# Kernel optimization log

Hardware: AMD Instinct MI355X
Metric: run time of the kernel (lower is better)

## Reference

```python
import jax, jax.numpy as jnp
import numpy as np

B, T, D = 2, 1024, 1024
H, HKV = 16, 4
HD = D // H            # 64, head dim
GROUPS = H // HKV      # 4
E, K, F = 32, 4, 256   # experts, top-k, expert hidden
FS = 2 * F             # shared expert hidden = n_shared_experts * expert_dim
ROPE_THETA = 500000.0


def rmsnorm(x, w, eps=1e-6):
    return x * jax.lax.rsqrt(jnp.mean(x * x, axis=-1, keepdims=True) + eps) * w


def apply_rope(x, cos, sin):
    # x: (B, T, H, HD); pairs of adjacent features form complex numbers
    xr = x.reshape(*x.shape[:-1], -1, 2)
    a, b = xr[..., 0], xr[..., 1]
    c = cos[None, :, None, :]
    s = sin[None, :, None, :]
    out = jnp.stack([a * c - b * s, a * s + b * c], axis=-1)
    return out.reshape(x.shape)


def setup_inputs():
    key = jax.random.key(0)
    ks = jax.random.split(key, 14)
    # RoPE phasors (real/imag of freqs_cis), shape (T, HD//2)
    inv = 1.0 / (ROPE_THETA ** (np.arange(0, HD, 2, dtype=np.float32) / HD))
    ang = np.arange(T, dtype=np.float32)[:, None] * inv[None, :]
    n = lambda k, shape, d: (jax.random.normal(k, shape, jnp.float32) / np.sqrt(d))
    return {
        "x": jax.random.normal(ks[0], (B, T, D), jnp.float32),
        "freqs_cos": jnp.asarray(np.cos(ang)),
        "freqs_sin": jnp.asarray(np.sin(ang)),
        "norm1_w": jnp.ones((D,), jnp.float32),
        "norm2_w": jnp.ones((D,), jnp.float32),
        "wq": n(ks[1], (D, H * HD), D),
        "wk": n(ks[2], (D, HKV * HD), D),
        "wv": n(ks[3], (D, HKV * HD), D),
        "wo": n(ks[4], (H * HD, D), H * HD),
        "router_w": n(ks[5], (D, E), D),
        "w_gate": n(ks[6], (E, D, F), D),
        "w_up": n(ks[7], (E, D, F), D),
        "w_down": n(ks[8], (E, F, D), F),
        "sh_gate": n(ks[9], (D, FS), D),
        "sh_up": n(ks[10], (D, FS), D),
        "sh_down": n(ks[11], (FS, D), FS),
    }


def reference(x, freqs_cos, freqs_sin, norm1_w, norm2_w, wq, wk, wv, wo,
              router_w, w_gate, w_up, w_down, sh_gate, sh_up, sh_down):
    # ---- GQA attention (pre-norm, residual), eval mode, causal ----
    h = rmsnorm(x, norm1_w)
    q = (h @ wq).reshape(B, T, H, HD)
    k = (h @ wk).reshape(B, T, HKV, HD)
    v = (h @ wv).reshape(B, T, HKV, HD)
    q = apply_rope(q, freqs_cos, freqs_sin)
    k = apply_rope(k, freqs_cos, freqs_sin)
    k = jnp.repeat(k, GROUPS, axis=2)   # (B, T, H, HD)
    v = jnp.repeat(v, GROUPS, axis=2)
    scores = jnp.einsum("bqhd,bkhd->bhqk", q, k) * (HD ** -0.5)
    causal = jnp.tril(jnp.ones((T, T), bool))
    scores = jnp.where(causal[None, None], scores, jnp.finfo(scores.dtype).min)
    probs = jax.nn.softmax(scores, axis=-1)
    attn = jnp.einsum("bhqk,bkhd->bqhd", probs, v).reshape(B, T, H * HD)
    x = x + attn @ wo

    # ---- top-K routed MoE SwiGLU FFN + shared expert (pre-norm, residual) ----
    h = rmsnorm(x, norm2_w).reshape(-1, D)              # (N, D)
    gate_scores = jax.nn.softmax(h @ router_w, axis=-1) # (N, E)
    top_vals, top_idx = jax.lax.top_k(gate_scores, K)   # (N, K)
    combine = jnp.sum(jax.nn.one_hot(top_idx, E, dtype=h.dtype) * top_vals[..., None], axis=1)  # (N, E)
    g = jnp.einsum("nd,edf->nef", h, w_gate)
    u = jnp.einsum("nd,edf->nef", h, w_up)
    hh = jax.nn.silu(g) * u * combine[:, :, None]       # combine-masked: only top-K experts contribute
    routed = jnp.einsum("nef,efd->nd", hh, w_down)
    shared = (jax.nn.silu(h @ sh_gate) * (h @ sh_up)) @ sh_down
    return x + (routed + shared).reshape(B, T, D)
```

## Files before the change

kernel.cpp:

```cpp
#include <hip/hip_runtime.h>

typedef unsigned short u16;
typedef _Float16 h8v __attribute__((ext_vector_type(8)));
typedef __attribute__((ext_vector_type(4))) float f4v;

#define DEV static __device__ __forceinline__

DEV u16 f2h(float f) {
  union { _Float16 h; u16 u; } v; v.h = (_Float16)f; return v.u;
}
DEV float h2f(u16 u) {
  union { u16 u; _Float16 h; } v; v.u = u; return (float)v.h;
}

DEV f4v mfma16h(h8v a, h8v b, f4v c) {
  return __builtin_amdgcn_mfma_f32_16x16x32_f16(a, b, c, 0, 0, 0);
}

__global__ __launch_bounds__(256) void prep_kernel(
    const float* __restrict__ wq, const float* __restrict__ wk,
    const float* __restrict__ wv, const float* __restrict__ wo,
    const float* __restrict__ shg, const float* __restrict__ shu,
    const float* __restrict__ shd,
    const float* __restrict__ wg, const float* __restrict__ wu,
    const float* __restrict__ wd,
    u16* __restrict__ wqkvT, u16* __restrict__ woT, u16* __restrict__ shguT,
    u16* __restrict__ shdT, u16* __restrict__ wguT, u16* __restrict__ wdT,
    const float* __restrict__ x, const float* __restrict__ n1w,
    u16* __restrict__ hH, int* __restrict__ counts) {
  int blk = blockIdx.x;
  if (blk < 7168) {
    const float* in; u16* out; int R, C, gx, gy; long long ozs; int base;
    if (blk < 256)       { in=wq;  out=wqkvT;                    R=1024; C=1024; gx=16; gy=16; ozs=0;        base=0; }
    else if (blk < 320)  { in=wk;  out=wqkvT+(size_t)1024*1024;  R=1024; C=256;  gx=4;  gy=16; ozs=0;        base=256; }
    else if (blk < 384)  { in=wv;  out=wqkvT+(size_t)1280*1024;  R=1024; C=256;  gx=4;  gy=16; ozs=0;        base=320; }
    else if (blk < 640)  { in=wo;  out=woT;                      R=1024; C=1024; gx=16; gy=16; ozs=0;        base=384; }
    else if (blk < 768)  { in=shg; out=shguT;                    R=1024; C=512;  gx=8;  gy=16; ozs=0;        base=640; }
    else if (blk < 896)  { in=shu; out=shguT+(size_t)512*1024;   R=1024; C=512;  gx=8;  gy=16; ozs=0;        base=768; }
    else if (blk < 1024) { in=shd; out=shdT;                     R=512;  C=1024; gx=16; gy=8;  ozs=0;        base=896; }
    else if (blk < 3072) { in=wg;  out=wguT;                     R=1024; C=256;  gx=4;  gy=16; ozs=512*1024; base=1024; }
    else if (blk < 5120) { in=wu;  out=wguT+(size_t)256*1024;    R=1024; C=256;  gx=4;  gy=16; ozs=512*1024; base=3072; }
    else                 { in=wd;  out=wdT;                      R=256;  C=1024; gx=16; gy=4;  ozs=256*1024; base=5120; }
    int i = blk - base;
    int bx = i % gx; int rem = i / gx; int by = rem % gy; int z = rem / gy;
    __shared__ float tile[64][65];
    const float* inp = in + (size_t)z * R * C;
    u16* op = out + (size_t)z * ozs;
    int c0 = bx * 64, r0 = by * 64;
    int tcol = (threadIdx.x & 15) * 4;
    int trow = threadIdx.x >> 4;
    #pragma unroll
    for (int p = 0; p < 4; ++p) {
      int row = trow + p*16;
      float4 v = *(const float4*)(inp + (size_t)(r0+row)*C + c0 + tcol);
      tile[row][tcol] = v.x; tile[row][tcol+1] = v.y;
      tile[row][tcol+2] = v.z; tile[row][tcol+3] = v.w;
    }
    __syncthreads();
    int tcol8 = (threadIdx.x & 7) * 8;
    int trow2 = threadIdx.x >> 3;
    #pragma unroll
    for (int p = 0; p < 2; ++p) {
      int c = trow2 + p*32;
      uint4 ov;
      ov.x = (unsigned)f2h(tile[tcol8+0][c]) | ((unsigned)f2h(tile[tcol8+1][c]) << 16);
      ov.y = (unsigned)f2h(tile[tcol8+2][c]) | ((unsigned)f2h(tile[tcol8+3][c]) << 16);
      ov.z = (unsigned)f2h(tile[tcol8+4][c]) | ((unsigned)f2h(tile[tcol8+5][c]) << 16);
      ov.w = (unsigned)f2h(tile[tcol8+6][c]) | ((unsigned)f2h(tile[tcol8+7][c]) << 16);
      *(uint4*)(op + (size_t)(c0+c)*R + r0 + tcol8) = ov;
    }
  } else if (blk < 9216) {
    int n = blk - 7168;
    int t = threadIdx.x;
    const float* xr = x + (size_t)n * 1024;
    float4 v = ((const float4*)xr)[t];
    float ss = v.x*v.x + v.y*v.y + v.z*v.z + v.w*v.w;
    #pragma unroll
    for (int o = 1; o < 64; o <<= 1) ss += __shfl_xor(ss, o, 64);
    __shared__ float wsum[4];
    if ((t & 63) == 0) wsum[t >> 6] = ss;
    __syncthreads();
    float tot = wsum[0] + wsum[1] + wsum[2] + wsum[3];
    float rs = rsqrtf(tot * (1.0f/1024.0f) + 1e-6f);
    float4 wv4 = ((const float4*)n1w)[t];
    ushort4 oh = { f2h(v.x*rs*wv4.x), f2h(v.y*rs*wv4.y),
                   f2h(v.z*rs*wv4.z), f2h(v.w*rs*wv4.w) };
    ((ushort4*)(hH + (size_t)n*1024))[t] = oh;
  } else {
    if (threadIdx.x < 32) counts[threadIdx.x] = 0;
  }
}

__global__ __launch_bounds__(256) void rmsnorm_kernel(const float* __restrict__ xin,
                                                      const float* __restrict__ w,
                                                      u16* __restrict__ outH,
                                                      float* __restrict__ outF) {
  int n = blockIdx.x;
  int t = threadIdx.x;
  const float* xr = xin + (size_t)n * 1024;
  float4 v = ((const float4*)xr)[t];
  float ss = v.x*v.x + v.y*v.y + v.z*v.z + v.w*v.w;
  #pragma unroll
  for (int o = 1; o < 64; o <<= 1) ss += __shfl_xor(ss, o, 64);
  __shared__ float wsum[4];
  if ((t & 63) == 0) wsum[t >> 6] = ss;
  __syncthreads();
  float tot = wsum[0] + wsum[1] + wsum[2] + wsum[3];
  float rs = rsqrtf(tot * (1.0f/1024.0f) + 1e-6f);
  float4 wv = ((const float4*)w)[t];
  float o0 = v.x*rs*wv.x, o1 = v.y*rs*wv.y, o2 = v.z*rs*wv.z, o3 = v.w*rs*wv.w;
  if (outF) {
    float4 of = {o0, o1, o2, o3};
    ((float4*)(outF + (size_t)n*1024))[t] = of;
  }
  ushort4 oh = { f2h(o0), f2h(o1), f2h(o2), f2h(o3) };
  ((ushort4*)(outH + (size_t)n*1024))[t] = oh;
}

__global__ __launch_bounds__(256) void gemm_kernel(
    const u16* __restrict__ Ah,
    const u16* __restrict__ Bh,
    float* __restrict__ C, u16* __restrict__ Ch16,
    const float* __restrict__ resid,
    const int* __restrict__ rowIdx, const int* __restrict__ counts,
    const int* __restrict__ offsets,
    int M, int N, int K, int strideBTe) {
  int M_ = M;
  const int* rIdx = rowIdx;
  int aOff = 0;
  if (counts) {
    int e = blockIdx.z;
    M_ = counts[e];
    if ((int)blockIdx.y * 64 >= M_) return;
    aOff = offsets[e];
    Bh += (size_t)e * strideBTe;
    if (Ch16) Ch16 += (size_t)aOff * N; else C += (size_t)aOff * N;
    if (rIdx) rIdx += aOff;
  }
  __shared__ u16 AtH[64*72];
  __shared__ u16 BtH[64*72];

  int tid = threadIdx.x;
  int wid = tid >> 6, lane = tid & 63;
  int lo16 = lane & 15, hi4 = lane >> 4;
  int m0 = blockIdx.y * 64, n0 = blockIdx.x * 64;
  int srow = tid >> 2, sseg = (tid & 3) * 16;

  int am = m0 + srow;
  int arow;
  if (counts) {
    int mm = (am < M_) ? am : (M_ - 1);
    arow = rIdx ? rIdx[mm] : (aOff + mm);
  } else {
    arow = am;
  }
  const u16* aPH = Ah + (size_t)arow * K;
  const u16* bPH = Bh + (size_t)(n0 + srow) * K;

  uint4 a0r, a1r, b0r, b1r;
  #define GLOAD(kb) { \
    a0r = *(const uint4*)(aPH + (kb) + sseg); a1r = *(const uint4*)(aPH + (kb) + sseg + 8); \
    b0r = *(const uint4*)(bPH + (kb) + sseg); b1r = *(const uint4*)(bPH + (kb) + sseg + 8); }
  #define GSTORE() { \
    *(uint4*)&AtH[srow*72 + sseg] = a0r; *(uint4*)&AtH[srow*72 + sseg + 8] = a1r; \
    *(uint4*)&BtH[srow*72 + sseg] = b0r; *(uint4*)&BtH[srow*72 + sseg + 8] = b1r; }

  f4v acc[4];
  #pragma unroll
  for (int j = 0; j < 4; ++j) { acc[j][0]=0.f; acc[j][1]=0.f; acc[j][2]=0.f; acc[j][3]=0.f; }

  GLOAD(0); GSTORE();
  for (int kb = 0; kb < K; kb += 64) {
    __syncthreads();
    if (kb + 64 < K) GLOAD(kb + 64);
    int ar = wid*16 + lo16;
    h8v ah0 = *(const h8v*)&AtH[ar*72 + 8*hi4];
    h8v ah1 = *(const h8v*)&AtH[ar*72 + 32 + 8*hi4];
    #pragma unroll
    for (int j = 0; j < 4; ++j) {
      int br = j*16 + lo16;
      h8v bh0 = *(const h8v*)&BtH[br*72 + 8*hi4];
      h8v bh1 = *(const h8v*)&BtH[br*72 + 32 + 8*hi4];
      acc[j] = mfma16h(ah0, bh0, acc[j]);
      acc[j] = mfma16h(ah1, bh1, acc[j]);
    }
    __syncthreads();
    if (kb + 64 < K) GSTORE();
  }
  #undef GLOAD
  #undef GSTORE
  #pragma unroll
  for (int r = 0; r < 4; ++r) {
    int rg = m0 + wid*16 + 4*hi4 + r;
    if (rg < M_) {
      size_t rb = (size_t)rg * N;
      #pragma unroll
      for (int j = 0; j < 4; ++j) {
        int cg = n0 + j*16 + lo16;
        float v = acc[j][r];
        if (resid) v += resid[rb + cg];
        if (Ch16) Ch16[rb + cg] = f2h(v);
        else      C[rb + cg] = v;
      }
    }
  }
}

__global__ __launch_bounds__(256) void rope_vtrans_kernel(
    const u16* __restrict__ src,
    const float* __restrict__ fc, const float* __restrict__ fs,
    u16* __restrict__ qOut, u16* __restrict__ kOut, u16* __restrict__ vOut) {
  int blk = blockIdx.x;
  if (blk < 5120) {
    int NH, colOff; u16* outH; int base;
    if (blk < 4096) { NH = 16; colOff = 0; outH = qOut; base = blk; }
    else            { NH = 4;  colOff = 1024; outH = kOut; base = blk - 4096; }
    int idx = base * 256 + threadIdx.x;
    int i = idx & 31; int tmp = idx >> 5;
    int hh = tmp % NH; int bt = tmp / NH;
    if (bt >= 2048) return;
    int t = bt & 1023, b = bt >> 10;
    const u16* sp = src + (size_t)bt * 1536 + colOff + hh*64 + 2*i;
    float a = h2f(sp[0]), bb = h2f(sp[1]);
    float c = fc[t*32 + i], s = fs[t*32 + i];
    float o0 = a*c - bb*s, o1 = a*s + bb*c;
    size_t o = (((size_t)(b*NH + hh))*1024 + t)*64 + 2*i;
    outH[o] = f2h(o0); outH[o+1] = f2h(o1);
  } else {
    int idx = (blk - 5120) * 256 + threadIdx.x;
    if (idx >= 2*4*64*1024) return;
    int t = idx & 1023; int tmp = idx >> 10;
    int hd = tmp & 63; int kv = (tmp >> 6) & 3; int b = tmp >> 8;
    vOut[idx] = src[(size_t)(b*1024 + t) * 1536 + 1280 + kv*64 + hd];
  }
}

__global__ __launch_bounds__(256) void attn_kernel(
    const u16* __restrict__ Qh,
    const u16* __restrict__ Kh_,
    const u16* __restrict__ Vh_,
    u16* __restrict__ Oh) {
  int b = blockIdx.z, h = blockIdx.y;
  int qb = (b == 0) ? (int)blockIdx.x : (15 - (int)blockIdx.x);
  int kv = h >> 2;
  size_t qoff = ((size_t)(b*16 + h)) * 65536;
  size_t koff = ((size_t)(b*4 + kv)) * 65536;

  __shared__ u16 KtH[64*72], VtH[64*72];
  __shared__ u16 PtH[4][16*72];

  int tid = threadIdx.x, wid = tid >> 6, lane = tid & 63;
  int lo16 = lane & 15, hi4 = lane >> 4;
  int srow = tid >> 2, sseg = (tid & 3) * 16;

  int qrow = qb*64 + wid*16 + lo16;
  const u16* qbh_ = Qh + qoff + (size_t)qrow*64;
  h8v qh0 = *(const h8v*)(qbh_ + 8*hi4);
  h8v qh1 = *(const h8v*)(qbh_ + 32 + 8*hi4);

  const u16* Kh = Kh_ + koff;
  const u16* Vh = Vh_ + koff;

  uint4 kh0r, kh1r, vh0r, vh1r;
  #define LOADT(kb) { \
    const u16* kh = Kh + (size_t)((kb)*64 + srow)*64 + sseg; \
    const u16* vh = Vh + (size_t)srow*1024 + (kb)*64 + sseg; \
    kh0r = *(const uint4*)(kh); kh1r = *(const uint4*)(kh + 8); \
    vh0r = *(const uint4*)(vh); vh1r = *(const uint4*)(vh + 8); }
  #define STORET() { \
    *(uint4*)&KtH[srow*72 + sseg]     = kh0r; *(uint4*)&KtH[srow*72 + sseg + 8] = kh1r; \
    *(uint4*)&VtH[srow*72 + sseg]     = vh0r; *(uint4*)&VtH[srow*72 + sseg + 8] = vh1r; }

  f4v oacc[4];
  #pragma unroll
  for (int j = 0; j < 4; ++j) { oacc[j][0]=0.f; oacc[j][1]=0.f; oacc[j][2]=0.f; oacc[j][3]=0.f; }
  float mrow[4] = {-1e30f, -1e30f, -1e30f, -1e30f};
  float lrow[4] = {0.f, 0.f, 0.f, 0.f};
  int qmy = qb*64 + wid*16 + 4*hi4;
  u16* PwH = PtH[wid];

  const float SC = 0.125f * 1.44269504088896f;

  LOADT(0); STORET();
  for (int kblk = 0; kblk <= qb; ++kblk) {
    __syncthreads();
    if (kblk < qb) LOADT(kblk + 1);

    f4v sfr[4];
    __builtin_amdgcn_s_setprio(1);
    #pragma unroll
    for (int j = 0; j < 4; ++j) {
      int kr = j*16 + lo16;
      h8v kh0 = *(const h8v*)&KtH[kr*72 + 8*hi4];
      h8v kh1 = *(const h8v*)&KtH[kr*72 + 32 + 8*hi4];
      f4v s; s[0]=0.f; s[1]=0.f; s[2]=0.f; s[3]=0.f;
      s = mfma16h(qh0, kh0, s);
      s = mfma16h(qh1, kh1, s);
      sfr[j] = s;
    }
    __builtin_amdgcn_s_setprio(0);

    bool diag = (kblk == qb);
    float scl[4];
    #pragma unroll
    for (int r = 0; r < 4; ++r) {
      int qr = qmy + r;
      #pragma unroll
      for (int j = 0; j < 4; ++j) {
        float v = sfr[j][r] * SC;
        if (diag) {
          int kc = kblk*64 + j*16 + lo16;
          v = (kc > qr) ? -1e30f : v;
        }
        sfr[j][r] = v;
      }
      float mx = fmaxf(fmaxf(sfr[0][r], sfr[1][r]), fmaxf(sfr[2][r], sfr[3][r]));
      #pragma unroll
      for (int o = 1; o < 16; o <<= 1) mx = fmaxf(mx, __shfl_xor(mx, o, 64));
      float mnew = fmaxf(mrow[r], mx);
      scl[r] = exp2f(mrow[r] - mnew);
      mrow[r] = mnew;
      float sum = 0.f;
      #pragma unroll
      for (int j = 0; j < 4; ++j) {
        float pv = exp2f(sfr[j][r] - mnew);
        sfr[j][r] = pv;
        sum += pv;
      }
      #pragma unroll
      for (int o = 1; o < 16; o <<= 1) sum += __shfl_xor(sum, o, 64);
      lrow[r] = lrow[r] * scl[r] + sum;
    }
    #pragma unroll
    for (int j = 0; j < 4; ++j) {
      #pragma unroll
      for (int r = 0; r < 4; ++r) oacc[j][r] *= scl[r];
    }

    #pragma unroll
    for (int r = 0; r < 4; ++r) {
      #pragma unroll
      for (int j = 0; j < 4; ++j) {
        PwH[(4*hi4 + r)*72 + j*16 + lo16] = f2h(sfr[j][r]);
      }
    }
    asm volatile("s_waitcnt lgkmcnt(0)" ::: "memory");
    h8v ph0 = *(const h8v*)&PwH[lo16*72 + 8*hi4];
    h8v ph1 = *(const h8v*)&PwH[lo16*72 + 32 + 8*hi4];

    __builtin_amdgcn_s_setprio(1);
    #pragma unroll
    for (int j = 0; j < 4; ++j) {
      int vr = j*16 + lo16;
      h8v vh0 = *(const h8v*)&VtH[vr*72 + 8*hi4];
      h8v vh1 = *(const h8v*)&VtH[vr*72 + 32 + 8*hi4];
      oacc[j] = mfma16h(ph0, vh0, oacc[j]);
      oacc[j] = mfma16h(ph1, vh1, oacc[j]);
    }
    __builtin_amdgcn_s_setprio(0);

    __syncthreads();
    if (kblk < qb) STORET();
  }
  #undef LOADT
  #undef STORET

  #pragma unroll
  for (int r = 0; r < 4; ++r) {
    float inv = 1.f / lrow[r];
    int tq = qb*64 + wid*16 + 4*hi4 + r;
    size_t base = ((size_t)(b*1024 + tq))*1024 + h*64;
    #pragma unroll
    for (int j = 0; j < 4; ++j) {
      Oh[base + j*16 + lo16] = f2h(oacc[j][r] * inv);
    }
  }
}

__global__ __launch_bounds__(256) void router_kernel(const float* __restrict__ h2,
                                                     const float* __restrict__ rw,
                                                     int* __restrict__ topIdx, float* __restrict__ topW,
                                                     int* __restrict__ counts) {
  __shared__ float hs[2][1024];
  __shared__ float part[4][32];
  __shared__ int hist[32];
  int t = threadIdx.x;
  int row0 = blockIdx.x * 2;
  if (t < 32) hist[t] = 0;

  {
    const float4* hsrc = (const float4*)(h2 + (size_t)row0 * 1024);
    float4* hdst = (float4*)&hs[0][0];
    hdst[t] = hsrc[t];
    hdst[t + 256] = hsrc[t + 256];
  }
  __syncthreads();

  int e = t & 31, g = t >> 5;
  int r = g >> 2, q = g & 3;
  const float* hp = &hs[r][q*256];
  const float* rp = rw + (size_t)(q*256)*32 + e;
  float b0 = 0.f, b1 = 0.f, b2 = 0.f, b3 = 0.f;
  #pragma unroll 16
  for (int d = 0; d < 256; d += 4) {
    b0 += hp[d+0] * rp[(d+0)*32];
    b1 += hp[d+1] * rp[(d+1)*32];
    b2 += hp[d+2] * rp[(d+2)*32];
    b3 += hp[d+3] * rp[(d+3)*32];
  }
  float pq = (b0 + b1) + (b2 + b3);
  pq += __shfl_xor(pq, 32, 64);
  int w = t >> 6;
  if ((t & 63) < 32) part[w][e] = pq;
  __syncthreads();

  if ((w & 1) == 0 && (t & 63) < 32) {
    float lg = part[w][e] + part[w+1][e];
    float mx = lg;
    #pragma unroll
    for (int o = 1; o < 32; o <<= 1) mx = fmaxf(mx, __shfl_xor(mx, o, 64));
    float ex = expf(lg - mx);
    float sm = ex;
    #pragma unroll
    for (int o = 1; o < 32; o <<= 1) sm += __shfl_xor(sm, o, 64);
    float prob = ex / sm;

    float pv = prob; int pi = e;
    int myRow = row0 + (w >> 1);
    for (int k = 0; k < 4; ++k) {
      float bv = pv; int bi = pi;
      #pragma unroll
      for (int o = 1; o < 32; o <<= 1) {
        float ov = __shfl_xor(bv, o, 64); int oi = __shfl_xor(bi, o, 64);
        if (ov > bv || (ov == bv && oi < bi)) { bv = ov; bi = oi; }
      }
      if (e == 0) {
        topIdx[myRow*4 + k] = bi; topW[myRow*4 + k] = bv;
        atomicAdd(&hist[bi], 1);
      }
      if (pi == bi) pv = -1.f;
    }
  }
  __syncthreads();
  if (t < 32 && hist[t] > 0) atomicAdd(&counts[t], hist[t]);
}

__global__ __launch_bounds__(256) void scan_scatter_kernel(
    const int* __restrict__ counts, int* __restrict__ offsets,
    const int* __restrict__ topIdx, const float* __restrict__ topW,
    int* __restrict__ rows, float* __restrict__ wtp, int* __restrict__ pslot) {
  __shared__ int cur[32];
  int t = threadIdx.x;
  if (t == 0) {
    int acc = 0;
    for (int e = 0; e < 32; ++e) { offsets[e] = acc; cur[e] = acc; acc += counts[e]; }
    offsets[32] = acc;
  }
  __syncthreads();
  for (int i = t; i < 8192; i += 256) {
    int e = topIdx[i];
    int slot = atomicAdd(&cur[e], 1);
    rows[slot] = i >> 2;
    wtp[slot] = topW[i];
    pslot[i] = slot;
  }
}

__global__ __launch_bounds__(256) void silu_mul_kernel(const u16* __restrict__ gu,
                                                       const float* __restrict__ wtp,
                                                       u16* __restrict__ out, int lg, int total) {
  int i = blockIdx.x * 256 + threadIdx.x;
  if (i >= total) return;
  int halfN = 1 << lg;
  int slot = i >> lg, e = i & (halfN - 1);
  size_t base = (size_t)slot * (2*halfN);
  float gv = h2f(gu[base + e]);
  float uv = h2f(gu[base + halfN + e]);
  float s = gv / (1.f + expf(-gv));
  float r = s * uv;
  if (wtp) r *= wtp[slot];
  out[i] = f2h(r);
}

__global__ __launch_bounds__(256) void final_kernel(const float* __restrict__ x1, const u16* __restrict__ shOut,
                                                    const u16* __restrict__ pairOut, const int* __restrict__ pslot,
                                                    float* __restrict__ out) {
  int n = blockIdx.x;
  int t = threadIdx.x;
  int s0 = pslot[n*4], s1 = pslot[n*4+1], s2 = pslot[n*4+2], s3 = pslot[n*4+3];
  float4 a  = ((const float4*)(x1 + (size_t)n*1024))[t];
  ushort4 sh = ((const ushort4*)(shOut + (size_t)n*1024))[t];
  ushort4 p0 = ((const ushort4*)(pairOut + (size_t)s0*1024))[t];
  ushort4 p1 = ((const ushort4*)(pairOut + (size_t)s1*1024))[t];
  ushort4 p2 = ((const ushort4*)(pairOut + (size_t)s2*1024))[t];
  ushort4 p3 = ((const ushort4*)(pairOut + (size_t)s3*1024))[t];
  float4 o;
  o.x = a.x + h2f(sh.x) + h2f(p0.x) + h2f(p1.x) + h2f(p2.x) + h2f(p3.x);
  o.y = a.y + h2f(sh.y) + h2f(p0.y) + h2f(p1.y) + h2f(p2.y) + h2f(p3.y);
  o.z = a.z + h2f(sh.z) + h2f(p0.z) + h2f(p1.z) + h2f(p2.z) + h2f(p3.z);
  o.w = a.w + h2f(sh.w) + h2f(p0.w) + h2f(p1.w) + h2f(p2.w) + h2f(p3.w);
  ((float4*)(out + (size_t)n*1024))[t] = o;
}

extern "C" void kernel_launch(void* const* d_in, const int* in_sizes, int n_in,
                              void* d_out, int out_size, void* d_ws, size_t ws_size,
                              hipStream_t stream) {
  const float* x   = (const float*)d_in[0];
  const float* fc  = (const float*)d_in[1];
  const float* fs  = (const float*)d_in[2];
  const float* n1w = (const float*)d_in[3];
  const float* n2w = (const float*)d_in[4];
  const float* wq  = (const float*)d_in[5];
  const float* wk  = (const float*)d_in[6];
  const float* wv  = (const float*)d_in[7];
  const float* wo  = (const float*)d_in[8];
  const float* rw  = (const float*)d_in[9];
  const float* wg  = (const float*)d_in[10];
  const float* wu  = (const float*)d_in[11];
  const float* wd  = (const float*)d_in[12];
  const float* shg = (const float*)d_in[13];
  const float* shu = (const float*)d_in[14];
  const float* shd = (const float*)d_in[15];
  float* out = (float*)d_out;
  (void)in_sizes; (void)n_in; (void)out_size;

  char* p = (char*)d_ws;
  auto alloc = [&](size_t n) { char* r = p; p += (n + 255) & ~(size_t)255; return r; };

  u16* wqkvT  = (u16*)alloc((size_t)1536*1024*2);
  u16* woT    = (u16*)alloc((size_t)1024*1024*2);
  u16* shguT  = (u16*)alloc((size_t)1024*1024*2);
  u16* shdT   = (u16*)alloc((size_t)1024*512*2);
  u16* wguT   = (u16*)alloc((size_t)32*512*1024*2);
  u16* wdT    = (u16*)alloc((size_t)32*1024*256*2);
  u16* hH     = (u16*)alloc((size_t)2048*1024*2);
  float* x1   = (float*)alloc((size_t)2048*1024*4);
  float* h2f_ = (float*)alloc((size_t)2048*1024*4);
  u16* h2b    = (u16*)alloc((size_t)2048*1024*2);
  u16* pairGU = (u16*)alloc((size_t)8192*512*2);
  u16* actb   = (u16*)alloc((size_t)8192*256*2);
  u16* sgu    = (u16*)alloc((size_t)2048*1024*2);
  u16* sactb  = (u16*)alloc((size_t)2048*512*2);
  u16* shOut  = (u16*)alloc((size_t)2048*1024*2);
  int* topIdx = (int*)alloc(2048*4*4);
  float* topW = (float*)alloc(2048*4*4);
  int* counts = (int*)alloc(32*4);
  int* offsets = (int*)alloc(33*4);
  int* rows   = (int*)alloc(8192*4);
  float* wtp  = (float*)alloc(8192*4);
  int* pslot  = (int*)alloc(8192*4);
  char* regionStart = p;
  u16* qkvh = (u16*)alloc((size_t)2048*1536*2);
  u16* qbh = (u16*)alloc((size_t)2048*1024*2);
  u16* kbh = (u16*)alloc((size_t)524288*2);
  u16* vth = (u16*)alloc((size_t)524288*2);
  u16* attnH = (u16*)alloc((size_t)2048*1024*2);
  u16* pairOut = (u16*)regionStart;
  {
    size_t regionBytes = (size_t)8192*1024*2;
    if ((size_t)(p - regionStart) < regionBytes) p = regionStart + regionBytes;
  }

  size_t needed = (size_t)(p - (char*)d_ws);
  if (needed > ws_size) return;

  dim3 blk(256);
  prep_kernel<<<9217, blk, 0, stream>>>(
      wq, wk, wv, wo, shg, shu, shd, wg, wu, wd,
      wqkvT, woT, shguT, shdT, wguT, wdT,
      x, n1w, hH, counts);
  gemm_kernel<<<dim3(24, 32), blk, 0, stream>>>(hH, wqkvT, nullptr, qkvh,
      nullptr, nullptr, nullptr, nullptr, 2048, 1536, 1024, 0);
  rope_vtrans_kernel<<<7168, blk, 0, stream>>>(qkvh, fc, fs, qbh, kbh, vth);
  attn_kernel<<<dim3(16,16,2), blk, 0, stream>>>(qbh, kbh, vth, attnH);
  gemm_kernel<<<dim3(16, 32), blk, 0, stream>>>(attnH, woT, x1, nullptr,
      x, nullptr, nullptr, nullptr, 2048, 1024, 1024, 0);
  rmsnorm_kernel<<<2048, blk, 0, stream>>>(x1, n2w, h2b, h2f_);
  router_kernel<<<1024, blk, 0, stream>>>(h2f_, rw, topIdx, topW, counts);
  scan_scatter_kernel<<<1, blk, 0, stream>>>(counts, offsets, topIdx, topW, rows, wtp, pslot);
  gemm_kernel<<<dim3(16, 32), blk, 0, stream>>>(h2b, shguT, nullptr, sgu,
      nullptr, nullptr, nullptr, nullptr, 2048, 1024, 1024, 0);
  silu_mul_kernel<<<4096, blk, 0, stream>>>(sgu, nullptr, sactb, 9, 2048*512);
  gemm_kernel<<<dim3(16, 32), blk, 0, stream>>>(sactb, shdT, nullptr, shOut,
      nullptr, nullptr, nullptr, nullptr, 2048, 1024, 512, 0);
  gemm_kernel<<<dim3(8, 32, 32), blk, 0, stream>>>(h2b, wguT, nullptr, pairGU,
      nullptr, rows, counts, offsets, 0, 512, 1024, 512*1024);
  silu_mul_kernel<<<8192, blk, 0, stream>>>(pairGU, wtp, actb, 8, 8192*256);
  gemm_kernel<<<dim3(16, 32, 32), blk, 0, stream>>>(actb, wdT, nullptr, pairOut,
      nullptr, nullptr, counts, offsets, 0, 1024, 256, 1024*256);
  final_kernel<<<2048, blk, 0, stream>>>(x1, shOut, pairOut, pslot, out);
}
```

Before: 245.8 us.

## Interleave gate/up weight columns and fuse SiLU-mul into GEMM epilogue

```diff
diff --git a/kernel.cpp b/kernel.cpp
--- a/kernel.cpp
+++ b/kernel.cpp
@@ -31,16 +31,17 @@
   int blk = blockIdx.x;
   if (blk < 7168) {
     const float* in; u16* out; int R, C, gx, gy; long long ozs; int base;
-    if (blk < 256)       { in=wq;  out=wqkvT;                    R=1024; C=1024; gx=16; gy=16; ozs=0;        base=0; }
-    else if (blk < 320)  { in=wk;  out=wqkvT+(size_t)1024*1024;  R=1024; C=256;  gx=4;  gy=16; ozs=0;        base=256; }
-    else if (blk < 384)  { in=wv;  out=wqkvT+(size_t)1280*1024;  R=1024; C=256;  gx=4;  gy=16; ozs=0;        base=320; }
-    else if (blk < 640)  { in=wo;  out=woT;                      R=1024; C=1024; gx=16; gy=16; ozs=0;        base=384; }
-    else if (blk < 768)  { in=shg; out=shguT;                    R=1024; C=512;  gx=8;  gy=16; ozs=0;        base=640; }
-    else if (blk < 896)  { in=shu; out=shguT+(size_t)512*1024;   R=1024; C=512;  gx=8;  gy=16; ozs=0;        base=768; }
-    else if (blk < 1024) { in=shd; out=shdT;                     R=512;  C=1024; gx=16; gy=8;  ozs=0;        base=896; }
-    else if (blk < 3072) { in=wg;  out=wguT;                     R=1024; C=256;  gx=4;  gy=16; ozs=512*1024; base=1024; }
-    else if (blk < 5120) { in=wu;  out=wguT+(size_t)256*1024;    R=1024; C=256;  gx=4;  gy=16; ozs=512*1024; base=3072; }
-    else                 { in=wd;  out=wdT;                      R=256;  C=1024; gx=16; gy=4;  ozs=256*1024; base=5120; }
+    int rmul, radd;
+    if (blk < 256)       { in=wq;  out=wqkvT;                    R=1024; C=1024; gx=16; gy=16; ozs=0;        base=0;    rmul=1; radd=0; }
+    else if (blk < 320)  { in=wk;  out=wqkvT+(size_t)1024*1024;  R=1024; C=256;  gx=4;  gy=16; ozs=0;        base=256;  rmul=1; radd=0; }
+    else if (blk < 384)  { in=wv;  out=wqkvT+(size_t)1280*1024;  R=1024; C=256;  gx=4;  gy=16; ozs=0;        base=320;  rmul=1; radd=0; }
+    else if (blk < 640)  { in=wo;  out=woT;                      R=1024; C=1024; gx=16; gy=16; ozs=0;        base=384;  rmul=1; radd=0; }
+    else if (blk < 768)  { in=shg; out=shguT;                    R=1024; C=512;  gx=8;  gy=16; ozs=0;        base=640;  rmul=2; radd=0; }
+    else if (blk < 896)  { in=shu; out=shguT;                    R=1024; C=512;  gx=8;  gy=16; ozs=0;        base=768;  rmul=2; radd=1; }
+    else if (blk < 1024) { in=shd; out=shdT;                     R=512;  C=1024; gx=16; gy=8;  ozs=0;        base=896;  rmul=1; radd=0; }
+    else if (blk < 3072) { in=wg;  out=wguT;                     R=1024; C=256;  gx=4;  gy=16; ozs=512*1024; base=1024; rmul=2; radd=0; }
+    else if (blk < 5120) { in=wu;  out=wguT;                     R=1024; C=256;  gx=4;  gy=16; ozs=512*1024; base=3072; rmul=2; radd=1; }
+    else                 { in=wd;  out=wdT;                      R=256;  C=1024; gx=16; gy=4;  ozs=256*1024; base=5120; rmul=1; radd=0; }
     int i = blk - base;
     int bx = i % gx; int rem = i / gx; int by = rem % gy; int z = rem / gy;
     __shared__ float tile[64][65];
@@ -67,7 +68,7 @@
       ov.y = (unsigned)f2h(tile[tcol8+2][c]) | ((unsigned)f2h(tile[tcol8+3][c]) << 16);
       ov.z = (unsigned)f2h(tile[tcol8+4][c]) | ((unsigned)f2h(tile[tcol8+5][c]) << 16);
       ov.w = (unsigned)f2h(tile[tcol8+6][c]) | ((unsigned)f2h(tile[tcol8+7][c]) << 16);
-      *(uint4*)(op + (size_t)(c0+c)*R + r0 + tcol8) = ov;
+      *(uint4*)(op + (size_t)((c0+c)*rmul + radd)*R + r0 + tcol8) = ov;
     }
   } else if (blk < 9216) {
     int n = blk - 7168;
@@ -121,6 +122,7 @@
     const u16* __restrict__ Ah,
     const u16* __restrict__ Bh,
     float* __restrict__ C, u16* __restrict__ Ch16,
+    u16* __restrict__ Csilu, const float* __restrict__ wtpP,
     const float* __restrict__ resid,
     const int* __restrict__ rowIdx, const int* __restrict__ counts,
     const int* __restrict__ offsets,
@@ -134,7 +136,10 @@
     if ((int)blockIdx.y * 64 >= M_) return;
     aOff = offsets[e];
     Bh += (size_t)e * strideBTe;
-    if (Ch16) Ch16 += (size_t)aOff * N; else C += (size_t)aOff * N;
+    if (Csilu)      Csilu += (size_t)aOff * (N >> 1);
+    else if (Ch16)  Ch16  += (size_t)aOff * N;
+    else            C     += (size_t)aOff * N;
+    if (wtpP) wtpP += aOff;
     if (rIdx) rIdx += aOff;
   }
   __shared__ u16 AtH[64*72];
@@ -193,14 +198,30 @@
   for (int r = 0; r < 4; ++r) {
     int rg = m0 + wid*16 + 4*hi4 + r;
     if (rg < M_) {
-      size_t rb = (size_t)rg * N;
-      #pragma unroll
-      for (int j = 0; j < 4; ++j) {
-        int cg = n0 + j*16 + lo16;
-        float v = acc[j][r];
-        if (resid) v += resid[rb + cg];
-        if (Ch16) Ch16[rb + cg] = f2h(v);
-        else      C[rb + cg] = v;
+      if (Csilu) {
+        size_t rb = (size_t)rg * (N >> 1);
+        #pragma unroll
+        for (int j = 0; j < 4; ++j) {
+          float own = acc[j][r];
+          float oth = __shfl_xor(own, 1, 64);
+          if ((lo16 & 1) == 0) {
+            float sg = own / (1.f + expf(-own));
+            float res = sg * oth;
+            if (wtpP) res *= wtpP[rg];
+            int cg = n0 + j*16 + lo16;
+            Csilu[rb + (cg >> 1)] = f2h(res);
+          }
+        }
+      } else {
+        size_t rb = (size_t)rg * N;
+        #pragma unroll
+        for (int j = 0; j < 4; ++j) {
+          int cg = n0 + j*16 + lo16;
+          float v = acc[j][r];
+          if (resid) v += resid[rb + cg];
+          if (Ch16) Ch16[rb + cg] = f2h(v);
+          else      C[rb + cg] = v;
+        }
       }
     }
   }
@@ -466,22 +487,6 @@
   }
 }
 
-__global__ __launch_bounds__(256) void silu_mul_kernel(const u16* __restrict__ gu,
-                                                       const float* __restrict__ wtp,
-                                                       u16* __restrict__ out, int lg, int total) {
-  int i = blockIdx.x * 256 + threadIdx.x;
-  if (i >= total) return;
-  int halfN = 1 << lg;
-  int slot = i >> lg, e = i & (halfN - 1);
-  size_t base = (size_t)slot * (2*halfN);
-  float gv = h2f(gu[base + e]);
-  float uv = h2f(gu[base + halfN + e]);
-  float s = gv / (1.f + expf(-gv));
-  float r = s * uv;
-  if (wtp) r *= wtp[slot];
-  out[i] = f2h(r);
-}
-
 __global__ __launch_bounds__(256) void final_kernel(const float* __restrict__ x1, const u16* __restrict__ shOut,
                                                     const u16* __restrict__ pairOut, const int* __restrict__ pslot,
                                                     float* __restrict__ out) {
@@ -537,9 +542,7 @@
   float* x1   = (float*)alloc((size_t)2048*1024*4);
   float* h2f_ = (float*)alloc((size_t)2048*1024*4);
   u16* h2b    = (u16*)alloc((size_t)2048*1024*2);
-  u16* pairGU = (u16*)alloc((size_t)8192*512*2);
   u16* actb   = (u16*)alloc((size_t)8192*256*2);
-  u16* sgu    = (u16*)alloc((size_t)2048*1024*2);
   u16* sactb  = (u16*)alloc((size_t)2048*512*2);
   u16* shOut  = (u16*)alloc((size_t)2048*1024*2);
   int* topIdx = (int*)alloc(2048*4*4);
@@ -569,24 +572,22 @@
       wq, wk, wv, wo, shg, shu, shd, wg, wu, wd,
       wqkvT, woT, shguT, shdT, wguT, wdT,
       x, n1w, hH, counts);
-  gemm_kernel<<<dim3(24, 32), blk, 0, stream>>>(hH, wqkvT, nullptr, qkvh,
+  gemm_kernel<<<dim3(24, 32), blk, 0, stream>>>(hH, wqkvT, nullptr, qkvh, nullptr, nullptr,
       nullptr, nullptr, nullptr, nullptr, 2048, 1536, 1024, 0);
   rope_vtrans_kernel<<<7168, blk, 0, stream>>>(qkvh, fc, fs, qbh, kbh, vth);
   attn_kernel<<<dim3(16,16,2), blk, 0, stream>>>(qbh, kbh, vth, attnH);
-  gemm_kernel<<<dim3(16, 32), blk, 0, stream>>>(attnH, woT, x1, nullptr,
+  gemm_kernel<<<dim3(16, 32), blk, 0, stream>>>(attnH, woT, x1, nullptr, nullptr, nullptr,
       x, nullptr, nullptr, nullptr, 2048, 1024, 1024, 0);
   rmsnorm_kernel<<<2048, blk, 0, stream>>>(x1, n2w, h2b, h2f_);
   router_kernel<<<1024, blk, 0, stream>>>(h2f_, rw, topIdx, topW, counts);
   scan_scatter_kernel<<<1, blk, 0, stream>>>(counts, offsets, topIdx, topW, rows, wtp, pslot);
-  gemm_kernel<<<dim3(16, 32), blk, 0, stream>>>(h2b, shguT, nullptr, sgu,
+  gemm_kernel<<<dim3(16, 32), blk, 0, stream>>>(h2b, shguT, nullptr, nullptr, sactb, nullptr,
       nullptr, nullptr, nullptr, nullptr, 2048, 1024, 1024, 0);
-  silu_mul_kernel<<<4096, blk, 0, stream>>>(sgu, nullptr, sactb, 9, 2048*512);
-  gemm_kernel<<<dim3(16, 32), blk, 0, stream>>>(sactb, shdT, nullptr, shOut,
+  gemm_kernel<<<dim3(16, 32), blk, 0, stream>>>(sactb, shdT, nullptr, shOut, nullptr, nullptr,
       nullptr, nullptr, nullptr, nullptr, 2048, 1024, 512, 0);
-  gemm_kernel<<<dim3(8, 32, 32), blk, 0, stream>>>(h2b, wguT, nullptr, pairGU,
+  gemm_kernel<<<dim3(8, 32, 32), blk, 0, stream>>>(h2b, wguT, nullptr, nullptr, actb, wtp,
       nullptr, rows, counts, offsets, 0, 512, 1024, 512*1024);
-  silu_mul_kernel<<<8192, blk, 0, stream>>>(pairGU, wtp, actb, 8, 8192*256);
-  gemm_kernel<<<dim3(16, 32, 32), blk, 0, stream>>>(actb, wdT, nullptr, pairOut,
+  gemm_kernel<<<dim3(16, 32, 32), blk, 0, stream>>>(actb, wdT, nullptr, pairOut, nullptr, nullptr,
       nullptr, nullptr, counts, offsets, 0, 1024, 256, 1024*256);
   final_kernel<<<2048, blk, 0, stream>>>(x1, shOut, pairOut, pslot, out);
 }
```

Measured after the change: 240.8 us (median of 2 runs). 1.02x faster.
